# Optimization experiments

Measured on AMD Instinct MI355X. Metric: run time of the kernel, lower is better.

Reference implementation:

```python
import jax, jax.numpy as jnp
import numpy as np

M, IN, OUT = 8192, 4096, 4096
BITWIDTH = 7


def psto_shift_int32(x, shift):
    """Pseudo-stochastic right-shift of int32 x by `shift` bits -> int8.
    Faithful to PstoShiftInt32: floor-divide, derive a pseudo random number
    from the low half of the remainder, compare against the high half."""
    pow_s = jnp.left_shift(jnp.int32(1), shift)
    rt = jnp.floor_divide(x, pow_s)
    prob = jnp.abs(x - rt * pow_s)
    half_pow = jnp.left_shift(jnp.int32(1), shift // 2)
    qp = jnp.floor_divide(prob, half_pow)
    prn = prob - qp * half_pow
    prn = jnp.where(shift % 2 == 1, prn * 2, prn)
    dec = jnp.where(qp <= prn, jnp.int32(0), jnp.int32(1)) * jnp.sign(x)
    return jnp.clip(rt + dec, -127, 127).astype(jnp.int8)


def range_bitwidth(x):
    # RangeEstimate: ceil(log2(max|x|)), 0 if all-zero (torch also goes via float)
    m = jnp.max(jnp.abs(x)).astype(jnp.float32)
    return jnp.where(m == 0, jnp.int32(0), jnp.ceil(jnp.log2(m)).astype(jnp.int32))


def act_calc(acc, exp_in):
    """Shift int32 accumulator back to int8 and track the block exponent."""
    bw = range_bitwidth(acc)
    shift = bw - BITWIDTH
    # shift>1 -> shift by `shift`; shift==1 -> shift by 2; else -> plain int8 cast
    eff = jnp.where(shift > 1, shift, jnp.where(shift == 1, jnp.int32(2), jnp.int32(0)))
    rounded = psto_shift_int32(acc, jnp.maximum(eff, 0))
    out = jnp.where(eff > 0, rounded, acc.astype(jnp.int8))  # int8 cast wraps, as in torch
    exp_out = (exp_in + eff).astype(jnp.int8)
    return out, exp_out


def setup_inputs() -> dict:
    key = jax.random.key(0)
    k1, k2 = jax.random.split(key)
    # int8-valued tensors kept in int32 containers for the matmul accumulate
    act_in = jax.random.randint(k1, (M, IN), -127, 128, dtype=jnp.int32)
    weight = jax.random.randint(k2, (OUT, IN), -127, 128, dtype=jnp.int32)
    return {"act_in": act_in, "exp_in": -6, "weight": weight, "weight_exp": -9}


def reference(act_in, exp_in, weight, weight_exp):
    # the roundoff4 padding in the original is a no-op)
    acc = jnp.matmul(act_in, weight.T)  # [M, OUT] int32
    act_out, exp_out = act_calc(acc, jnp.int32(exp_in) + jnp.int32(weight_exp))
    return act_out, exp_out
```

## Files before the change

### kernel.cpp

```cpp
#include <hip/hip_runtime.h>
#include <stdint.h>
#include <math.h>

#define M_DIM 8192
#define N_DIM 4096
#define K_DIM 4096
#define BITWIDTH 7

#define BM 128
#define BN 128
#define BK 64

using i32x4  = __attribute__((ext_vector_type(4)))  int;
using i32x16 = __attribute__((ext_vector_type(16))) int;

__global__ __launch_bounds__(256) void pack_both_kernel(
        const int* __restrict__ act, const int* __restrict__ wt,
        uint32_t* __restrict__ act8, uint32_t* __restrict__ w8) {
    const int ACT_N8 = (M_DIM * K_DIM) / 8;
    int i = blockIdx.x * blockDim.x + threadIdx.x;
    const int* src;
    uint32_t* dst;
    if (i < ACT_N8) { src = act; dst = act8; }
    else            { src = wt;  dst = w8;  i -= ACT_N8; }
    int4 a = ((const int4*)src)[2 * i];
    int4 b = ((const int4*)src)[2 * i + 1];
    uint32_t p0 = (uint32_t)(a.x & 0xFF) | ((uint32_t)(a.y & 0xFF) << 8)
                | ((uint32_t)(a.z & 0xFF) << 16) | ((uint32_t)(a.w & 0xFF) << 24);
    uint32_t p1 = (uint32_t)(b.x & 0xFF) | ((uint32_t)(b.y & 0xFF) << 8)
                | ((uint32_t)(b.z & 0xFF) << 16) | ((uint32_t)(b.w & 0xFF) << 24);
    ((uint2*)dst)[i] = make_uint2(p0, p1);
}

__device__ __forceinline__ void gload_lds16(const int8_t* g, int8_t* lds) {
    __builtin_amdgcn_global_load_lds(
        (__attribute__((address_space(1))) void*)g,
        (__attribute__((address_space(3))) void*)lds,
        16, 0, 0);
}

__global__ __launch_bounds__(256) void gemm_i8(const int8_t* __restrict__ A8,
                                               const int8_t* __restrict__ B8,
                                               int* __restrict__ C,
                                               int* __restrict__ maxabs) {
    __shared__ __align__(16) int8_t As[BM * BK];
    __shared__ __align__(16) int8_t Bs[BN * BK];
    __shared__ int wmaxs[4];

    const int tid  = threadIdx.x;
    const int wave = tid >> 6;
    const int lane = tid & 63;

    const int row0 = blockIdx.y * BM;
    const int col0 = blockIdx.x * BN;

    const int wm = (wave >> 1) * 64;
    const int wn = (wave & 1) * 64;

    i32x16 acc[2][2];
#pragma unroll
    for (int i = 0; i < 2; ++i)
#pragma unroll
        for (int j = 0; j < 2; ++j)
            acc[i][j] = (i32x16)(0);

    const int lr  = lane >> 2;
    const int lcb = (lane & 3) << 4;
    const int ra  = wave * 32;

    const int8_t* ag = A8 + (size_t)(row0 + ra + lr) * K_DIM + lcb;
    const int8_t* bg = B8 + (size_t)(col0 + ra + lr) * K_DIM + lcb;

    const int fr = lane & 31;
    const int fk = (lane >> 5) << 4;

    for (int k0 = 0; k0 < K_DIM; k0 += BK) {
        __syncthreads();
        gload_lds16(ag + k0,                        As + ra * BK);
        gload_lds16(ag + k0 + (size_t)16 * K_DIM,   As + (ra + 16) * BK);
        gload_lds16(bg + k0,                        Bs + ra * BK);
        gload_lds16(bg + k0 + (size_t)16 * K_DIM,   Bs + (ra + 16) * BK);
        __syncthreads();

        i32x4 af[2][2], bf[2][2];
#pragma unroll
        for (int i = 0; i < 2; ++i)
#pragma unroll
            for (int kk = 0; kk < 2; ++kk) {
                af[i][kk] = *(const i32x4*)(As + (wm + i * 32 + fr) * BK + kk * 32 + fk);
                bf[i][kk] = *(const i32x4*)(Bs + (wn + i * 32 + fr) * BK + kk * 32 + fk);
            }

#pragma unroll
        for (int kk = 0; kk < 2; ++kk)
#pragma unroll
            for (int i = 0; i < 2; ++i)
#pragma unroll
                for (int j = 0; j < 2; ++j)
                    acc[i][j] = __builtin_amdgcn_mfma_i32_32x32x32_i8(
                        af[i][kk], bf[j][kk], acc[i][j], 0, 0, 0);
    }

    int mymax = 0;
    const int ccol = lane & 31;
    const int rbase = (lane >> 5) << 2;
#pragma unroll
    for (int i = 0; i < 2; ++i) {
#pragma unroll
        for (int j = 0; j < 2; ++j) {
            int* p = C + (size_t)(row0 + wm + i * 32) * N_DIM
                       + (col0 + wn + j * 32 + ccol);
#pragma unroll
            for (int r = 0; r < 16; ++r) {
                int row = (r & 3) + 8 * (r >> 2) + rbase;
                int v = acc[i][j][r];
                p[(size_t)row * N_DIM] = v;
                int a = v < 0 ? -v : v;
                mymax = a > mymax ? a : mymax;
            }
        }
    }

#pragma unroll
    for (int off = 32; off > 0; off >>= 1) {
        int o = __shfl_down(mymax, off, 64);
        mymax = o > mymax ? o : mymax;
    }
    if (lane == 0) wmaxs[wave] = mymax;
    __syncthreads();
    if (tid == 0) {
        int bmx = wmaxs[0];
        for (int w = 1; w < 4; ++w) bmx = wmaxs[w] > bmx ? wmaxs[w] : bmx;
        atomicMax(maxabs, bmx);
    }
}

__device__ __forceinline__ int psto(int x, int eff) {
    if (eff > 0) {
        int rt   = x >> eff;
        int prob = x & ((1 << eff) - 1);
        int h    = eff >> 1;
        int qp   = prob >> h;
        int prn  = (prob & ((1 << h) - 1)) << (eff & 1);
        int sgn  = (x > 0) - (x < 0);
        int r    = rt + ((qp <= prn) ? 0 : sgn);
        r = r < -127 ? -127 : r;
        r = r > 127 ? 127 : r;
        return r;
    }
    return (int)(int8_t)x;
}

__global__ __launch_bounds__(256) void finalize_kernel(int* __restrict__ C,
        const int* __restrict__ maxabs,
        const int* __restrict__ exp_in,
        const int* __restrict__ wexp) {
    const int m = *maxabs;
    int bw = 0;
    if (m != 0) bw = (int)ceilf(log2f((float)m));
    const int shift = bw - BITWIDTH;
    const int eff = (shift > 1) ? shift : ((shift == 1) ? 2 : 0);

    const size_t idx = ((size_t)blockIdx.x * blockDim.x + threadIdx.x) * 8;
    int4 v0 = *(const int4*)(C + idx);
    int4 v1 = *(const int4*)(C + idx + 4);
    int4 o0, o1;
    o0.x = psto(v0.x, eff); o0.y = psto(v0.y, eff);
    o0.z = psto(v0.z, eff); o0.w = psto(v0.w, eff);
    o1.x = psto(v1.x, eff); o1.y = psto(v1.y, eff);
    o1.z = psto(v1.z, eff); o1.w = psto(v1.w, eff);
    *(int4*)(C + idx) = o0;
    *(int4*)(C + idx + 4) = o1;

    if (idx == 0) {
        C[(size_t)M_DIM * N_DIM] = (int)(int8_t)(exp_in[0] + wexp[0] + eff);
    }
}

extern "C" void kernel_launch(void* const* d_in, const int* in_sizes, int n_in,
                              void* d_out, int out_size, void* d_ws, size_t ws_size,
                              hipStream_t stream) {
    const int* act    = (const int*)d_in[0];
    const int* exp_in = (const int*)d_in[1];
    const int* wt     = (const int*)d_in[2];
    const int* wexp   = (const int*)d_in[3];

    int8_t* act8   = (int8_t*)d_ws;
    int8_t* w8     = act8 + (size_t)M_DIM * K_DIM;
    int*    maxabs = (int*)(w8 + (size_t)N_DIM * K_DIM);

    hipMemsetAsync(maxabs, 0, sizeof(int), stream);

    pack_both_kernel<<<24576, 256, 0, stream>>>(
        act, wt, (uint32_t*)act8, (uint32_t*)w8);

    int* C = (int*)d_out;
    dim3 grid(N_DIM / BN, M_DIM / BM);
    gemm_i8<<<grid, 256, 0, stream>>>(act8, w8, C, maxabs);

    finalize_kernel<<<((size_t)M_DIM * N_DIM / 8) / 256, 256, 0, stream>>>(
        C, maxabs, exp_in, wexp);
}
```

Before: 490.6 us.

## Double K tile to 128 with XOR-swizzled LDS layout, fold memset into pack

Raises BK from 64 to 128 so each main-loop iteration issues twice as many MFMAs per pair of barriers, halving the synchronisation count. It adds an XOR swizzle on the 16-byte chunk index for both the global-to-LDS loads and the fragment reads, meant to avoid LDS bank conflicts with the longer rows. It also drops the hipMemsetAsync by zeroing the max accumulator inside the pack kernel, saving one launch. LDS use doubles to 32 KB per block, which may lower occupancy.

```diff
diff --git a/kernel.cpp b/kernel.cpp
--- a/kernel.cpp
+++ b/kernel.cpp
@@ -9,14 +9,16 @@
 
 #define BM 128
 #define BN 128
-#define BK 64
+#define BK 128
 
 using i32x4  = __attribute__((ext_vector_type(4)))  int;
 using i32x16 = __attribute__((ext_vector_type(16))) int;
 
 __global__ __launch_bounds__(256) void pack_both_kernel(
         const int* __restrict__ act, const int* __restrict__ wt,
-        uint32_t* __restrict__ act8, uint32_t* __restrict__ w8) {
+        uint32_t* __restrict__ act8, uint32_t* __restrict__ w8,
+        int* __restrict__ maxabs) {
+    if (blockIdx.x == 0 && threadIdx.x == 0) *maxabs = 0;
     const int ACT_N8 = (M_DIM * K_DIM) / 8;
     int i = blockIdx.x * blockDim.x + threadIdx.x;
     const int* src;
@@ -64,46 +66,57 @@
         for (int j = 0; j < 2; ++j)
             acc[i][j] = (i32x16)(0);
 
-    const int lr  = lane >> 2;
-    const int lcb = (lane & 3) << 4;
-    const int ra  = wave * 32;
-
-    const int8_t* ag = A8 + (size_t)(row0 + ra + lr) * K_DIM + lcb;
-    const int8_t* bg = B8 + (size_t)(col0 + ra + lr) * K_DIM + lcb;
-
-    const int fr = lane & 31;
-    const int fk = (lane >> 5) << 4;
+    const int ra     = wave * 32;
+    const int rowoff = lane >> 3;
+    const int chk    = ((lane & 7) ^ rowoff) << 4;
+
+    const int8_t* ag = A8 + (size_t)(row0 + ra + rowoff) * K_DIM + chk;
+    const int8_t* bg = B8 + (size_t)(col0 + ra + rowoff) * K_DIM + chk;
+
+    const int fr  = lane & 31;
+    const int hl  = lane >> 5;
+    const int swz = fr & 7;
+    int aoff[2][4], boff[2][4];
+#pragma unroll
+    for (int kk = 0; kk < 4; ++kk) {
+        int c = kk * 2 + hl;
+        int co = ((c ^ swz) << 4);
+#pragma unroll
+        for (int i = 0; i < 2; ++i) {
+            aoff[i][kk] = (wm + i * 32 + fr) * BK + co;
+            boff[i][kk] = (wn + i * 32 + fr) * BK + co;
+        }
+    }
 
     for (int k0 = 0; k0 < K_DIM; k0 += BK) {
         __syncthreads();
-        gload_lds16(ag + k0,                        As + ra * BK);
-        gload_lds16(ag + k0 + (size_t)16 * K_DIM,   As + (ra + 16) * BK);
-        gload_lds16(bg + k0,                        Bs + ra * BK);
-        gload_lds16(bg + k0 + (size_t)16 * K_DIM,   Bs + (ra + 16) * BK);
+#pragma unroll
+        for (int g = 0; g < 4; ++g) {
+            gload_lds16(ag + k0 + (size_t)(8 * g) * K_DIM, As + (ra + 8 * g) * BK);
+            gload_lds16(bg + k0 + (size_t)(8 * g) * K_DIM, Bs + (ra + 8 * g) * BK);
+        }
         __syncthreads();
 
-        i32x4 af[2][2], bf[2][2];
-#pragma unroll
-        for (int i = 0; i < 2; ++i)
-#pragma unroll
-            for (int kk = 0; kk < 2; ++kk) {
-                af[i][kk] = *(const i32x4*)(As + (wm + i * 32 + fr) * BK + kk * 32 + fk);
-                bf[i][kk] = *(const i32x4*)(Bs + (wn + i * 32 + fr) * BK + kk * 32 + fk);
+#pragma unroll
+        for (int kk = 0; kk < 4; ++kk) {
+            i32x4 af[2], bf[2];
+#pragma unroll
+            for (int i = 0; i < 2; ++i) {
+                af[i] = *(const i32x4*)(As + aoff[i][kk]);
+                bf[i] = *(const i32x4*)(Bs + boff[i][kk]);
             }
-
-#pragma unroll
-        for (int kk = 0; kk < 2; ++kk)
 #pragma unroll
             for (int i = 0; i < 2; ++i)
 #pragma unroll
                 for (int j = 0; j < 2; ++j)
                     acc[i][j] = __builtin_amdgcn_mfma_i32_32x32x32_i8(
-                        af[i][kk], bf[j][kk], acc[i][j], 0, 0, 0);
+                        af[i], bf[j], acc[i][j], 0, 0, 0);
+        }
     }
 
     int mymax = 0;
     const int ccol = lane & 31;
-    const int rbase = (lane >> 5) << 2;
+    const int rbase = hl << 2;
 #pragma unroll
     for (int i = 0; i < 2; ++i) {
 #pragma unroll
@@ -189,10 +202,8 @@
     int8_t* w8     = act8 + (size_t)M_DIM * K_DIM;
     int*    maxabs = (int*)(w8 + (size_t)N_DIM * K_DIM);
 
-    hipMemsetAsync(maxabs, 0, sizeof(int), stream);
-
     pack_both_kernel<<<24576, 256, 0, stream>>>(
-        act, wt, (uint32_t*)act8, (uint32_t*)w8);
+        act, wt, (uint32_t*)act8, (uint32_t*)w8, maxabs);
 
     int* C = (int*)d_out;
     dim3 grid(N_DIM / BN, M_DIM / BM);
```

Result: faster. 448.5 us (-8.6%).
